# Optimization experiments

Measured on AMD Instinct MI355X. Metric: run time of the kernel, lower is better.

The kernel has to match this reference:

```python
import jax, jax.numpy as jnp
import numpy as np

NUM_GRAPHS = 512

def setup_inputs() -> dict:
    key = jax.random.key(0)
    ks = jax.random.split(key, 6)
    N, E, D = 100000, 1600000, 128
    x = jax.random.normal(ks[0], (N, D), dtype=jnp.float32)
    edge_index = jax.random.randint(ks[1], (2, E), 0, N, dtype=jnp.int64)
    batch = jnp.sort(jax.random.randint(ks[2], (N,), 0, NUM_GRAPHS, dtype=jnp.int64))
    scale = 1.0 / np.sqrt(D)
    Ws = jax.random.normal(ks[3], (4, D, D), dtype=jnp.float32) * scale
    bs = jnp.zeros((4, D), dtype=jnp.float32)
    Wl = jax.random.normal(ks[4], (D, 1), dtype=jnp.float32) * scale
    bl = jnp.zeros((1,), dtype=jnp.float32)
    return {"x": x, "edge_index": edge_index, "batch": batch,
            "Ws": Ws, "bs": bs, "Wl": Wl, "bl": bl}

def reference(x, edge_index, batch, Ws, bs, Wl, bl):
    N = x.shape[0]
    loops = jnp.arange(N, dtype=edge_index.dtype)
    # GCNConv: add self-loops, symmetric normalization D^{-1/2} A D^{-1/2}
    row = jnp.concatenate([edge_index[0], loops])  # source nodes
    col = jnp.concatenate([edge_index[1], loops])  # target nodes
    deg = jax.ops.segment_sum(jnp.ones_like(col, dtype=x.dtype), col, num_segments=N)
    dinv = jnp.where(deg > 0, jax.lax.rsqrt(jnp.maximum(deg, 1.0)), 0.0)
    norm = dinv[row] * dinv[col]  # [E+N]
    h = x
    for i in range(Ws.shape[0]):
        h = h @ Ws[i]                                   # [N, D]
        msg = h[row] * norm[:, None]                    # gather + scale, [E+N, D]
        h = jax.ops.segment_sum(msg, col, num_segments=N) + bs[i]
        h = jax.nn.relu(h)                              # dropout is identity in eval
    # global_mean_pool over graphs
    sums = jax.ops.segment_sum(h, batch, num_segments=NUM_GRAPHS)
    cnt = jax.ops.segment_sum(jnp.ones((N,), h.dtype), batch, num_segments=NUM_GRAPHS)
    pooled = sums / jnp.maximum(cnt, 1.0)[:, None]      # [G, D]
    return pooled @ Wl + bl                             # [G, 1]
```

## Files before the change

### kernel.cpp

```cpp
#include <hip/hip_runtime.h>


constexpr int D = 128;
constexpr int NGRAPH = 512;
constexpr int CHUNK = 4096;
constexpr int BSH = 9;
constexpr int OP = 136;

typedef __attribute__((ext_vector_type(8))) short bf16x8;
typedef __attribute__((ext_vector_type(4))) float f32x4;

__device__ __forceinline__ float bf2f(unsigned short b) {
    return __uint_as_float(((unsigned int)b) << 16);
}
__device__ __forceinline__ unsigned short f2bf(float f) {
    unsigned int u = __float_as_uint(f);
    u += 0x7FFFu + ((u >> 16) & 1u);
    return (unsigned short)(u >> 16);
}

__global__ __launch_bounds__(256) void setup_all(
        const float4* __restrict__ x4, ushort4* __restrict__ hb, int n4, int CB,
        const float* __restrict__ W, unsigned short* __restrict__ Wt,
        const int* __restrict__ ec, int E, int* __restrict__ bucketCnt) {
    __shared__ int h[256];
    const int t = threadIdx.x;
    const int b = blockIdx.x;
    if (b < CB) {
        int i = b * 256 + t;
        if (i < n4) {
            float4 v = x4[i];
            ushort4 o;
            o.x = f2bf(v.x); o.y = f2bf(v.y); o.z = f2bf(v.z); o.w = f2bf(v.w);
            hb[i] = o;
        }
    } else if (b < CB + 256) {
        int idx = (b - CB) * 256 + t;
        int i = idx >> 14;
        int rem = idx & 16383;
        int k = rem >> 7, c = rem & 127;
        Wt[(i << 14) + c * 128 + k] = f2bf(W[idx]);
    } else {
        h[t] = 0;
        __syncthreads();
        const int e0 = (b - CB - 256) * CHUNK;
        const int cnt = min(CHUNK, E - e0);
        for (int i = t; i < cnt; i += 256) atomicAdd(&h[ec[e0 + i] >> BSH], 1);
        __syncthreads();
        if (h[t]) atomicAdd(&bucketCnt[t], h[t]);
    }
}

__global__ __launch_bounds__(256) void bucket_scan(const int* __restrict__ bucketCnt,
                                                   int* __restrict__ bucketBase,
                                                   int* __restrict__ globCursor) {
    __shared__ int s[256];
    const int t = threadIdx.x;
    int v = bucketCnt[t];
    s[t] = v; __syncthreads();
    for (int off = 1; off < 256; off <<= 1) {
        int x = (t >= off) ? s[t - off] : 0;
        __syncthreads();
        s[t] += x;
        __syncthreads();
    }
    int excl = s[t] - v;
    bucketBase[t] = excl;
    globCursor[t] = excl;
}

__global__ __launch_bounds__(256) void scatter_pairs(const int* __restrict__ er,
                                                     const int* __restrict__ ec, int E,
                                                     int* __restrict__ globCursor,
                                                     int2* __restrict__ pairs) {
    __shared__ int h[256], lbase[256], cur[256], segd[256], s[256];
    __shared__ int2 stage[CHUNK];
    const int t = threadIdx.x;
    const int e0 = blockIdx.x * CHUNK;
    const int cnt = min(CHUNK, E - e0);

    h[t] = 0;
    __syncthreads();
    for (int i = t; i < cnt; i += 256) atomicAdd(&h[ec[e0 + i] >> BSH], 1);
    __syncthreads();
    int v = h[t];
    s[t] = v; __syncthreads();
    for (int off = 1; off < 256; off <<= 1) {
        int x = (t >= off) ? s[t - off] : 0;
        __syncthreads();
        s[t] += x;
        __syncthreads();
    }
    lbase[t] = s[t] - v;
    cur[t] = s[t] - v;
    segd[t] = atomicAdd(&globCursor[t], v) - lbase[t];
    __syncthreads();
    for (int i = t; i < cnt; i += 256) {
        int c = ec[e0 + i];
        int b = c >> BSH;
        int p = atomicAdd(&cur[b], 1);
        stage[p] = make_int2(er[e0 + i], c);
    }
    __syncthreads();
    for (int i = t; i < cnt; i += 256) {
        int2 pr = stage[i];
        int b = pr.y >> BSH;
        pairs[segd[b] + i] = pr;
    }
}

__global__ __launch_bounds__(256) void fill_csr(const int2* __restrict__ pairs,
                                                const int* __restrict__ bucketBase,
                                                const int* __restrict__ bucketCnt,
                                                int N, int E, int NBUCK,
                                                int* __restrict__ rowptr,
                                                float* __restrict__ dinv,
                                                int* __restrict__ srcs) {
    __shared__ int hist[512], lofs[512], s[256];
    const int t = threadIdx.x;
    const int b = blockIdx.x;
    const int c0 = b << BSH;
    const int base = bucketBase[b];
    const int cnt = bucketCnt[b];
    const int2* pp = pairs + base;

    hist[t] = 0; hist[t + 256] = 0;
    __syncthreads();
    for (int i = t; i < cnt; i += 256) atomicAdd(&hist[pp[i].y - c0], 1);
    __syncthreads();
    int a0 = hist[2 * t], a1 = hist[2 * t + 1];
    s[t] = a0 + a1; __syncthreads();
    for (int off = 1; off < 256; off <<= 1) {
        int x = (t >= off) ? s[t - off] : 0;
        __syncthreads();
        s[t] += x;
        __syncthreads();
    }
    int excl = s[t] - (a0 + a1);
    lofs[2 * t] = excl;
    lofs[2 * t + 1] = excl + a0;
    __syncthreads();
    const int nn = min(512, N - c0);
    for (int i = t; i < nn; i += 256) {
        rowptr[c0 + i] = base + lofs[i];
        dinv[c0 + i] = rsqrtf((float)hist[i] + 1.0f);
    }
    if (b == NBUCK - 1 && t == 0) rowptr[N] = E;
    __syncthreads();
    for (int i = t; i < cnt; i += 256) {
        int2 pr = pp[i];
        int p = atomicAdd(&lofs[pr.y - c0], 1);
        srcs[base + p] = pr.x;
    }
}

__global__ __launch_bounds__(256) void pull_agg(const int* __restrict__ rowptr,
                                                const int* __restrict__ srcs,
                                                const float* __restrict__ dinv,
                                                const unsigned short* __restrict__ H,
                                                unsigned short* __restrict__ Pb, int N) {
    int node = blockIdx.x * 8 + (threadIdx.x >> 5);
    int lane = threadIdx.x & 31;
    if (node >= N) return;
    int j = rowptr[node], end = rowptr[node + 1];
    const ushort4* H2 = (const ushort4*)H;
    float sn = dinv[node];
    ushort4 hs = H2[(size_t)node * 32 + lane];
    float4 acc = make_float4(sn * bf2f(hs.x), sn * bf2f(hs.y),
                             sn * bf2f(hs.z), sn * bf2f(hs.w));
    for (; j + 8 <= end; j += 8) {
        int r[8]; float s[8]; ushort4 h[8];
#pragma unroll
        for (int t = 0; t < 8; ++t) r[t] = srcs[j + t];
#pragma unroll
        for (int t = 0; t < 8; ++t) s[t] = dinv[r[t]];
#pragma unroll
        for (int t = 0; t < 8; ++t) h[t] = H2[(size_t)r[t] * 32 + lane];
#pragma unroll
        for (int t = 0; t < 8; ++t) {
            acc.x += s[t] * bf2f(h[t].x); acc.y += s[t] * bf2f(h[t].y);
            acc.z += s[t] * bf2f(h[t].z); acc.w += s[t] * bf2f(h[t].w);
        }
    }
    for (; j < end; ++j) {
        int r0 = srcs[j];
        float s0 = dinv[r0];
        ushort4 h0 = H2[(size_t)r0 * 32 + lane];
        acc.x += s0 * bf2f(h0.x); acc.y += s0 * bf2f(h0.y);
        acc.z += s0 * bf2f(h0.z); acc.w += s0 * bf2f(h0.w);
    }
    ushort4 o;
    o.x = f2bf(sn * acc.x); o.y = f2bf(sn * acc.y);
    o.z = f2bf(sn * acc.z); o.w = f2bf(sn * acc.w);
    ((ushort4*)Pb)[(size_t)node * 32 + lane] = o;
}

__global__ __launch_bounds__(256) void gemm_mfma(const unsigned short* __restrict__ Pb,
                                                 const unsigned short* __restrict__ Wt,
                                                 const float* __restrict__ bias,
                                                 unsigned short* __restrict__ Hn,
                                                 float* __restrict__ dots,
                                                 const float* __restrict__ Wl,
                                                 int writeDots) {
    __shared__ __align__(16) unsigned short u[4][32 * OP];
    const int wave = threadIdx.x >> 6;
    const int lane = threadIdx.x & 63;
    const int row16 = lane & 15;
    const int quad = lane >> 4;
    const int r0 = blockIdx.x * 128 + wave * 32;
    unsigned short* U = u[wave];

    {
        const int lr = lane >> 1, hf = lane & 1;
        const bf16x8* g = (const bf16x8*)(Pb + (size_t)(r0 + lr) * 128);
        bf16x8* l = (bf16x8*)(U + lr * 128);
#pragma unroll
        for (int i = 0; i < 8; ++i) {
            int c = hf * 8 + i;
            l[c ^ (lr & 15)] = g[c];
        }
    }
    __syncthreads();

    bf16x8 a0[4], a1[4];
#pragma unroll
    for (int kc = 0; kc < 4; ++kc) {
        const int ph = (kc * 4 + quad) ^ row16;
        a0[kc] = *(const bf16x8*)(U + row16 * 128 + ph * 8);
        a1[kc] = *(const bf16x8*)(U + (16 + row16) * 128 + ph * 8);
    }
    __syncthreads();

    float rd0[4] = {0.f, 0.f, 0.f, 0.f}, rd1[4] = {0.f, 0.f, 0.f, 0.f};
#pragma unroll
    for (int ct = 0; ct < 8; ++ct) {
        const int col = ct * 16 + row16;
        const bf16x8* wc = (const bf16x8*)(Wt + (size_t)col * 128);
        f32x4 acc0 = {0.f, 0.f, 0.f, 0.f}, acc1 = {0.f, 0.f, 0.f, 0.f};
#pragma unroll
        for (int kc = 0; kc < 4; ++kc) {
            const bf16x8 wf = wc[kc * 4 + quad];
            acc0 = __builtin_amdgcn_mfma_f32_16x16x32_bf16(a0[kc], wf, acc0, 0, 0, 0);
            acc1 = __builtin_amdgcn_mfma_f32_16x16x32_bf16(a1[kc], wf, acc1, 0, 0, 0);
        }
        const float bv = bias[col];
        if (writeDots) {
            const float wl = Wl[col];
#pragma unroll
            for (int i = 0; i < 4; ++i) {
                rd0[i] += fmaxf(acc0[i] + bv, 0.f) * wl;
                rd1[i] += fmaxf(acc1[i] + bv, 0.f) * wl;
            }
        } else {
#pragma unroll
            for (int i = 0; i < 4; ++i) {
                U[(quad * 4 + i) * OP + col] = f2bf(fmaxf(acc0[i] + bv, 0.f));
                U[(16 + quad * 4 + i) * OP + col] = f2bf(fmaxf(acc1[i] + bv, 0.f));
            }
        }
    }

    if (writeDots) {
#pragma unroll
        for (int m = 1; m < 16; m <<= 1)
#pragma unroll
            for (int i = 0; i < 4; ++i) {
                rd0[i] += __shfl_xor(rd0[i], m, 64);
                rd1[i] += __shfl_xor(rd1[i], m, 64);
            }
        if (row16 == 0) {
#pragma unroll
            for (int i = 0; i < 4; ++i) {
                dots[r0 + quad * 4 + i] = rd0[i];
                dots[r0 + 16 + quad * 4 + i] = rd1[i];
            }
        }
    } else {
        __syncthreads();
#pragma unroll
        for (int i = 0; i < 8; ++i) {
            int idx = i * 64 + lane;
            int row = idx >> 4, c8 = idx & 15;
            bf16x8 v = *(const bf16x8*)(U + row * OP + c8 * 8);
            *(bf16x8*)(Hn + (size_t)(r0 + row) * 128 + c8 * 8) = v;
        }
    }
}

__global__ __launch_bounds__(256) void pool_graphs(const float* __restrict__ dots,
                                                   const int* __restrict__ batch, int N,
                                                   const float* __restrict__ bl,
                                                   float* __restrict__ out) {
    __shared__ int bounds[2];
    __shared__ float red[4];
    const int g = blockIdx.x;
    const int t = threadIdx.x;
    if (t < 2) {
        int key = g + t;
        int lo = 0, hi = N;
        while (lo < hi) {
            int mid = (lo + hi) >> 1;
            if (batch[mid] < key) lo = mid + 1; else hi = mid;
        }
        bounds[t] = lo;
    }
    __syncthreads();
    const int lo = bounds[0], hi = bounds[1];
    float s = 0.f;
    for (int i = lo + t; i < hi; i += 256) s += dots[i];
#pragma unroll
    for (int off = 32; off > 0; off >>= 1) s += __shfl_down(s, off, 64);
    if ((t & 63) == 0) red[t >> 6] = s;
    __syncthreads();
    if (t == 0) {
        float tot = red[0] + red[1] + red[2] + red[3];
        int cnt = hi - lo;
        out[g] = tot / (float)(cnt > 0 ? cnt : 1) + bl[0];
    }
}

extern "C" void kernel_launch(void* const* d_in, const int* in_sizes, int n_in,
                              void* d_out, int out_size, void* d_ws, size_t ws_size,
                              hipStream_t stream) {
    const float* x     = (const float*)d_in[0];
    const int*   eidx  = (const int*)d_in[1];
    const int*   batch = (const int*)d_in[2];
    const float* Ws    = (const float*)d_in[3];
    const float* bs    = (const float*)d_in[4];
    const float* Wl    = (const float*)d_in[5];
    const float* bl    = (const float*)d_in[6];
    (void)n_in; (void)out_size;

    const int N = in_sizes[0] / D;
    const int E = in_sizes[1] / 2;
    const int* er = eidx;
    const int* ec = eidx + E;
    const int NBUCK = (N + 511) >> BSH;
    const int NCHUNK = (E + CHUNK - 1) / CHUNK;

    const int Npad = (N + 127) & ~127;
    const size_t hBytes = (size_t)Npad * D * sizeof(unsigned short);
    auto al = [](size_t v) { return (v + 255) & ~(size_t)255; };
    char* base = (char*)d_ws;
    size_t off = 0;

    unsigned short* Pb = (unsigned short*)base;  off = al(hBytes);
    int2* pairs = (int2*)Pb;
    int* bucketCnt  = (int*)(base + off);
    int* globCursor = bucketCnt + 256;
    off = al(off + 512 * sizeof(int));
    int*   bucketBase = (int*)(base + off);  off = al(off + 256 * sizeof(int));
    float* dinv   = (float*)(base + off);    off = al(off + (size_t)Npad * sizeof(float));
    float* dots   = (float*)(base + off);    off = al(off + (size_t)Npad * sizeof(float));
    int*   rowptr = (int*)(base + off);      off = al(off + (size_t)(Npad + 64) * sizeof(int));
    int*   srcs   = (int*)(base + off);      off = al(off + (size_t)E * sizeof(int));
    unsigned short* Wt = (unsigned short*)(base + off);   off = al(off + 4 * 128 * 128 * sizeof(unsigned short));
    unsigned short* Hb0 = (unsigned short*)(base + off);  off = al(off + hBytes);

    const bool twoBuf = ws_size >= off + hBytes;
    unsigned short* Hb1 = twoBuf ? (unsigned short*)(base + off)
                                 : (unsigned short*)d_in[0];
    unsigned short* hb[2] = { Hb0, Hb1 };

    hipMemsetAsync(bucketCnt, 0, 256 * sizeof(int), stream);
    const int n4 = N * D / 4;
    const int CB = (n4 + 255) / 256;
    setup_all<<<CB + 256 + NCHUNK, 256, 0, stream>>>((const float4*)x, (ushort4*)Hb0,
                                                     n4, CB, Ws, Wt, ec, E, bucketCnt);

    bucket_scan<<<1, 256, 0, stream>>>(bucketCnt, bucketBase, globCursor);
    scatter_pairs<<<NCHUNK, 256, 0, stream>>>(er, ec, E, globCursor, pairs);
    fill_csr<<<NBUCK, 256, 0, stream>>>(pairs, bucketBase, bucketCnt, N, E, NBUCK,
                                        rowptr, dinv, srcs);

    for (int i = 0; i < 4; ++i) {
        const unsigned short* Hc = hb[i & 1];
        unsigned short* Hn = hb[(i + 1) & 1];
        pull_agg<<<(N + 7) / 8, 256, 0, stream>>>(rowptr, srcs, dinv, Hc, Pb, N);
        gemm_mfma<<<Npad / 128, 256, 0, stream>>>(Pb, Wt + (size_t)i * D * D,
                                                  bs + (size_t)i * D, Hn, dots, Wl,
                                                  (i == 3) ? 1 : 0);
    }

    pool_graphs<<<NGRAPH, 256, 0, stream>>>(dots, batch, N, bl, (float*)d_out);
}
```

Measured before the change: 521.1 us.

## Fuse neighbor aggregation into MFMA GEMM kernel and pre-scale outputs by dinv

Merges the pull-aggregation kernel and the GEMM into one per-layer kernel, so aggregated rows are built directly in LDS instead of going through a global bf16 buffer. Layer outputs are now multiplied by the node's dinv before storage, which removes the per-edge dinv gather in later layers. In exchange, each wave aggregates 32 rows with 16 lanes per row using 8-wide loads, so a wave may serialize over uneven degrees. Grid size drops to N/128 blocks, which may reduce latency hiding for the irregular gathers. Workspace buffers are reassigned so the CSR pairs scratch now lives in the second H buffer.

```diff
diff --git a/kernel.cpp b/kernel.cpp
--- a/kernel.cpp
+++ b/kernel.cpp
@@ -154,54 +154,12 @@
     }
 }
 
-__global__ __launch_bounds__(256) void pull_agg(const int* __restrict__ rowptr,
-                                                const int* __restrict__ srcs,
-                                                const float* __restrict__ dinv,
-                                                const unsigned short* __restrict__ H,
-                                                unsigned short* __restrict__ Pb, int N) {
-    int node = blockIdx.x * 8 + (threadIdx.x >> 5);
-    int lane = threadIdx.x & 31;
-    if (node >= N) return;
-    int j = rowptr[node], end = rowptr[node + 1];
-    const ushort4* H2 = (const ushort4*)H;
-    float sn = dinv[node];
-    ushort4 hs = H2[(size_t)node * 32 + lane];
-    float4 acc = make_float4(sn * bf2f(hs.x), sn * bf2f(hs.y),
-                             sn * bf2f(hs.z), sn * bf2f(hs.w));
-    for (; j + 8 <= end; j += 8) {
-        int r[8]; float s[8]; ushort4 h[8];
-#pragma unroll
-        for (int t = 0; t < 8; ++t) r[t] = srcs[j + t];
-#pragma unroll
-        for (int t = 0; t < 8; ++t) s[t] = dinv[r[t]];
-#pragma unroll
-        for (int t = 0; t < 8; ++t) h[t] = H2[(size_t)r[t] * 32 + lane];
-#pragma unroll
-        for (int t = 0; t < 8; ++t) {
-            acc.x += s[t] * bf2f(h[t].x); acc.y += s[t] * bf2f(h[t].y);
-            acc.z += s[t] * bf2f(h[t].z); acc.w += s[t] * bf2f(h[t].w);
-        }
-    }
-    for (; j < end; ++j) {
-        int r0 = srcs[j];
-        float s0 = dinv[r0];
-        ushort4 h0 = H2[(size_t)r0 * 32 + lane];
-        acc.x += s0 * bf2f(h0.x); acc.y += s0 * bf2f(h0.y);
-        acc.z += s0 * bf2f(h0.z); acc.w += s0 * bf2f(h0.w);
-    }
-    ushort4 o;
-    o.x = f2bf(sn * acc.x); o.y = f2bf(sn * acc.y);
-    o.z = f2bf(sn * acc.z); o.w = f2bf(sn * acc.w);
-    ((ushort4*)Pb)[(size_t)node * 32 + lane] = o;
-}
-
-__global__ __launch_bounds__(256) void gemm_mfma(const unsigned short* __restrict__ Pb,
-                                                 const unsigned short* __restrict__ Wt,
-                                                 const float* __restrict__ bias,
-                                                 unsigned short* __restrict__ Hn,
-                                                 float* __restrict__ dots,
-                                                 const float* __restrict__ Wl,
-                                                 int writeDots) {
+__global__ __launch_bounds__(256, 4) void layer_fused(
+        const int* __restrict__ rowptr, const int* __restrict__ srcs,
+        const float* __restrict__ dinv, const unsigned short* __restrict__ H,
+        const unsigned short* __restrict__ Wt, const float* __restrict__ bias,
+        unsigned short* __restrict__ Hn, float* __restrict__ dots,
+        const float* __restrict__ Wl, int N, int preScaled, int writeDots) {
     __shared__ __align__(16) unsigned short u[4][32 * OP];
     const int wave = threadIdx.x >> 6;
     const int lane = threadIdx.x & 63;
@@ -209,15 +167,72 @@
     const int quad = lane >> 4;
     const int r0 = blockIdx.x * 128 + wave * 32;
     unsigned short* U = u[wave];
+    const bf16x8* H8 = (const bf16x8*)H;
 
     {
-        const int lr = lane >> 1, hf = lane & 1;
-        const bf16x8* g = (const bf16x8*)(Pb + (size_t)(r0 + lr) * 128);
-        bf16x8* l = (bf16x8*)(U + lr * 128);
-#pragma unroll
-        for (int i = 0; i < 8; ++i) {
-            int c = hf * 8 + i;
-            l[c ^ (lr & 15)] = g[c];
+        const int gl = row16;
+        const int rb = quad * 8;
+        for (int sstep = 0; sstep < 8; ++sstep) {
+            const int rt = rb + sstep;
+            const int row = r0 + rt;
+            float acc[8] = {0.f, 0.f, 0.f, 0.f, 0.f, 0.f, 0.f, 0.f};
+            float sn = 0.f;
+            if (row < N) {
+                sn = dinv[row];
+                int j = rowptr[row];
+                const int end = rowptr[row + 1];
+                bf16x8 hv = H8[(size_t)row * 16 + gl];
+                const float sf = preScaled ? 1.f : sn;
+#pragma unroll
+                for (int k = 0; k < 8; ++k) acc[k] = sf * bf2f((unsigned short)hv[k]);
+                if (preScaled) {
+                    for (; j + 8 <= end; j += 8) {
+                        int r[8]; bf16x8 h[8];
+#pragma unroll
+                        for (int t = 0; t < 8; ++t) r[t] = srcs[j + t];
+#pragma unroll
+                        for (int t = 0; t < 8; ++t) h[t] = H8[(size_t)r[t] * 16 + gl];
+#pragma unroll
+                        for (int t = 0; t < 8; ++t)
+#pragma unroll
+                            for (int k = 0; k < 8; ++k)
+                                acc[k] += bf2f((unsigned short)h[t][k]);
+                    }
+                    for (; j < end; ++j) {
+                        bf16x8 h0 = H8[(size_t)srcs[j] * 16 + gl];
+#pragma unroll
+                        for (int k = 0; k < 8; ++k)
+                            acc[k] += bf2f((unsigned short)h0[k]);
+                    }
+                } else {
+                    for (; j + 8 <= end; j += 8) {
+                        int r[8]; float sc[8]; bf16x8 h[8];
+#pragma unroll
+                        for (int t = 0; t < 8; ++t) r[t] = srcs[j + t];
+#pragma unroll
+                        for (int t = 0; t < 8; ++t) sc[t] = dinv[r[t]];
+#pragma unroll
+                        for (int t = 0; t < 8; ++t) h[t] = H8[(size_t)r[t] * 16 + gl];
+#pragma unroll
+                        for (int t = 0; t < 8; ++t)
+#pragma unroll
+                            for (int k = 0; k < 8; ++k)
+                                acc[k] += sc[t] * bf2f((unsigned short)h[t][k]);
+                    }
+                    for (; j < end; ++j) {
+                        int r00 = srcs[j];
+                        float s0 = dinv[r00];
+                        bf16x8 h0 = H8[(size_t)r00 * 16 + gl];
+#pragma unroll
+                        for (int k = 0; k < 8; ++k)
+                            acc[k] += s0 * bf2f((unsigned short)h0[k]);
+                    }
+                }
+            }
+            bf16x8 o;
+#pragma unroll
+            for (int k = 0; k < 8; ++k) o[k] = (short)f2bf(sn * acc[k]);
+            *(bf16x8*)(U + rt * 128 + ((gl ^ (rt & 15)) << 3)) = o;
         }
     }
     __syncthreads();
@@ -230,6 +245,17 @@
         a1[kc] = *(const bf16x8*)(U + (16 + row16) * 128 + ph * 8);
     }
     __syncthreads();
+
+    float dvA[4], dvB[4];
+    if (!writeDots) {
+#pragma unroll
+        for (int i = 0; i < 4; ++i) {
+            int ra = r0 + quad * 4 + i;
+            int rbg = ra + 16;
+            dvA[i] = (ra < N) ? dinv[ra] : 0.f;
+            dvB[i] = (rbg < N) ? dinv[rbg] : 0.f;
+        }
+    }
 
     float rd0[4] = {0.f, 0.f, 0.f, 0.f}, rd1[4] = {0.f, 0.f, 0.f, 0.f};
 #pragma unroll
@@ -254,8 +280,8 @@
         } else {
 #pragma unroll
             for (int i = 0; i < 4; ++i) {
-                U[(quad * 4 + i) * OP + col] = f2bf(fmaxf(acc0[i] + bv, 0.f));
-                U[(16 + quad * 4 + i) * OP + col] = f2bf(fmaxf(acc1[i] + bv, 0.f));
+                U[(quad * 4 + i) * OP + col] = f2bf(dvA[i] * fmaxf(acc0[i] + bv, 0.f));
+                U[(16 + quad * 4 + i) * OP + col] = f2bf(dvB[i] * fmaxf(acc1[i] + bv, 0.f));
             }
         }
     }
@@ -344,8 +370,7 @@
     char* base = (char*)d_ws;
     size_t off = 0;
 
-    unsigned short* Pb = (unsigned short*)base;  off = al(hBytes);
-    int2* pairs = (int2*)Pb;
+    unsigned short* Hb0 = (unsigned short*)base; off = al(hBytes);
     int* bucketCnt  = (int*)(base + off);
     int* globCursor = bucketCnt + 256;
     off = al(off + 512 * sizeof(int));
@@ -355,11 +380,11 @@
     int*   rowptr = (int*)(base + off);      off = al(off + (size_t)(Npad + 64) * sizeof(int));
     int*   srcs   = (int*)(base + off);      off = al(off + (size_t)E * sizeof(int));
     unsigned short* Wt = (unsigned short*)(base + off);   off = al(off + 4 * 128 * 128 * sizeof(unsigned short));
-    unsigned short* Hb0 = (unsigned short*)(base + off);  off = al(off + hBytes);
 
     const bool twoBuf = ws_size >= off + hBytes;
     unsigned short* Hb1 = twoBuf ? (unsigned short*)(base + off)
                                  : (unsigned short*)d_in[0];
+    int2* pairs = (int2*)Hb1;
     unsigned short* hb[2] = { Hb0, Hb1 };
 
     hipMemsetAsync(bucketCnt, 0, 256 * sizeof(int), stream);
@@ -376,10 +401,11 @@
     for (int i = 0; i < 4; ++i) {
         const unsigned short* Hc = hb[i & 1];
         unsigned short* Hn = hb[(i + 1) & 1];
-        pull_agg<<<(N + 7) / 8, 256, 0, stream>>>(rowptr, srcs, dinv, Hc, Pb, N);
-        gemm_mfma<<<Npad / 128, 256, 0, stream>>>(Pb, Wt + (size_t)i * D * D,
-                                                  bs + (size_t)i * D, Hn, dots, Wl,
-                                                  (i == 3) ? 1 : 0);
+        layer_fused<<<Npad / 128, 256, 0, stream>>>(rowptr, srcs, dinv, Hc,
+                                                    Wt + (size_t)i * D * D,
+                                                    bs + (size_t)i * D, Hn, dots, Wl,
+                                                    N, (i > 0) ? 1 : 0,
+                                                    (i == 3) ? 1 : 0);
     }
 
     pool_graphs<<<NGRAPH, 256, 0, stream>>>(dots, batch, N, bl, (float*)d_out);
```

After: 502.8 us. -3.5%, faster.
